# Optimization experiments

Measured on AMD Instinct MI355X. Metric: run time of the kernel, lower is better.

The kernel has to match this reference:

```python
import jax, jax.numpy as jnp
import numpy as np

G = 8          # n_games
D_IN = 512     # per-game input dim (equal for all games)
H1 = 1024
H2 = 1024
A = 128        # max_actions
B = 8192       # batch rows


def setup_inputs() -> dict:
    key = jax.random.key(0)
    ks = jax.random.split(key, 9)
    state = jax.random.normal(ks[0], (B, D_IN), dtype=jnp.float32)
    idx = jax.random.randint(ks[1], (B,), 0, G, dtype=jnp.int32)
    # per-game input linears: uniform(-1/sqrt(fan_in), 1/sqrt(fan_in))
    lim1 = 1.0 / np.sqrt(D_IN)
    W1 = jax.random.uniform(ks[2], (G, D_IN, H1), minval=-lim1, maxval=lim1, dtype=jnp.float32)
    b1 = jax.random.uniform(ks[3], (G, H1), minval=-lim1, maxval=lim1, dtype=jnp.float32)
    # shared linear
    lim2 = 1.0 / np.sqrt(H1)
    W2 = jax.random.uniform(ks[4], (H1, H2), minval=-lim2, maxval=lim2, dtype=jnp.float32)
    b2 = jax.random.uniform(ks[5], (H2,), minval=-lim2, maxval=lim2, dtype=jnp.float32)
    # per-game output heads: uniform(-0.003, 0.003)
    W3 = jax.random.uniform(ks[6], (G, H2, A), minval=-0.003, maxval=0.003, dtype=jnp.float32)
    b3 = jax.random.uniform(ks[7], (G, A), minval=-0.003, maxval=0.003, dtype=jnp.float32)
    return {"state": state, "idx": idx, "W1": W1, "b1": b1, "W2": W2, "b2": b2, "W3": W3, "b3": b3}


def reference(state, idx, W1, b1, W2, b2, W3, b3):
    # Torch code concatenates per-game groups in sorted-unique-idx order,
    # i.e. a stable permutation of rows by idx; reproduce exactly.
    perm = jnp.argsort(idx, stable=True)          # [B]
    s = state[perm]                               # [B, D_IN]
    g = idx[perm]                                 # [B] game of each permuted row
    # routed first layer: compute all games then gather per-row game
    h1_all = jnp.einsum('bd,gdh->bgh', s, W1) + b1            # [B, G, H1]
    h1 = jax.nn.relu(jnp.take_along_axis(h1_all, g[:, None, None], axis=1)[:, 0, :])  # [B, H1]
    h_f = jax.nn.relu(h1 @ W2 + b2)                            # [B, H2]
    a = jnp.tanh(jnp.einsum('bh,gha->bga', h_f, W3) + b3)      # [B, G, A]
    # NOTE: original gathers heads with the ORIGINAL (unpermuted) idx,
    # even though rows of `a` are in permuted order. Reproduce faithfully.
    out = jnp.take_along_axis(a, idx[:, None, None], axis=1)[:, 0, :]  # [B, A]
    return out
```

## Files before the change

kernel.cpp:

```cpp
#include <hip/hip_runtime.h>
#include <math.h>

#define G_GAMES 8
#define D_IN 512
#define H1 1024
#define H2 1024
#define A_DIM 128
#define B_ROWS 8192

typedef short bf16x8 __attribute__((ext_vector_type(8)));
typedef float f32x4 __attribute__((ext_vector_type(4)));

#define WS_OFF   0u
#define WS_PERM  256u
#define WS_SPERM 33280u
#define WS_W1T   (WS_SPERM + B_ROWS*D_IN*2u)
#define WS_W2T   (WS_W1T + G_GAMES*D_IN*H1*2u)
#define WS_W3T   (WS_W2T + (unsigned)H1*H2*2u)
#define WS_H1    (WS_W3T + G_GAMES*H2*A_DIM*2u)
#define WS_HF    WS_SPERM

__device__ __forceinline__ unsigned short f2bf(float x) {
  union { float f; unsigned int u; } v; v.f = x;
  unsigned int r = v.u + 0x7fffu + ((v.u >> 16) & 1u);
  return (unsigned short)(r >> 16);
}

__device__ __forceinline__ unsigned int cvt_pk_bf16(float lo, float hi) {
  unsigned int r;
  asm("v_cvt_pk_bf16_f32 %0, %1, %2" : "=v"(r) : "v"(lo), "v"(hi));
  return r;
}

__device__ __forceinline__ void async_load16(const void* gptr, void* ldsptr) {
  __builtin_amdgcn_global_load_lds(
      (const __attribute__((address_space(1))) unsigned int*)gptr,
      (__attribute__((address_space(3))) unsigned int*)ldsptr,
      16, 0, 0);
}

__device__ void sort_256(const int* __restrict__ idx, int* __restrict__ perm,
                         int* __restrict__ off) {
  __shared__ int wtot[4][9];
  __shared__ int wbase[4][9];
  __shared__ int offs[9];
  const int t = threadIdx.x, lane = t & 63, wave = t >> 6;
  int my[32];
#pragma unroll
  for (int i = 0; i < 8; ++i) {
    const int4 a = *(const int4*)(idx + t * 32 + i * 4);
    my[i*4+0] = a.x; my[i*4+1] = a.y; my[i*4+2] = a.z; my[i*4+3] = a.w;
  }
  int local[8];
#pragma unroll
  for (int g = 0; g < 8; ++g) {
    int c = 0;
#pragma unroll
    for (int i = 0; i < 32; ++i) c += (my[i] == g) ? 1 : 0;
    local[g] = c;
  }
  int incl[8];
#pragma unroll
  for (int g = 0; g < 8; ++g) {
    int v = local[g];
#pragma unroll
    for (int d = 1; d < 64; d <<= 1) {
      const int n = __shfl_up(v, d);
      if (lane >= d) v += n;
    }
    incl[g] = v;
  }
  if (lane == 63) {
#pragma unroll
    for (int g = 0; g < 8; ++g) wtot[wave][g] = incl[g];
  }
  __syncthreads();
  if (t < 8) {
    int s = 0;
#pragma unroll
    for (int w = 0; w < 4; ++w) { wbase[w][t] = s; s += wtot[w][t]; }
    wtot[0][t] = s;
  }
  __syncthreads();
  if (t == 0) {
    int s = 0;
#pragma unroll
    for (int g = 0; g < 8; ++g) { offs[g] = s; off[g] = s; s += wtot[0][g]; }
    offs[8] = s; off[8] = s;
  }
  __syncthreads();
#pragma unroll
  for (int g = 0; g < 8; ++g) {
    int sg = offs[g] + wbase[wave][g] + (incl[g] - local[g]);
#pragma unroll
    for (int i = 0; i < 32; ++i) {
      const bool m = (my[i] == g);
      if (m) perm[sg] = t * 32 + i;
      sg += m ? 1 : 0;
    }
  }
}

__device__ void trans_tile_ws(char* ldsbuf, const float* __restrict__ in,
                              unsigned short* __restrict__ out,
                              int R, int C, int xt, int yt, int z) {
  in  += (size_t)z * R * C;
  out += (size_t)z * R * C;
  unsigned short (*tl)[68] = (unsigned short(*)[68])ldsbuf;
  const int c0 = xt * 64, r0 = yt * 64;
  const int t = threadIdx.x;
#pragma unroll
  for (int pass = 0; pass < 4; ++pass) {
    const int id = pass * 256 + t;
    const int r = id >> 4, f4c = (id & 15) << 2;
    const float4 v = *(const float4*)(in + (size_t)(r0 + r) * C + c0 + f4c);
    uint2 w;
    w.x = cvt_pk_bf16(v.x, v.y);
    w.y = cvt_pk_bf16(v.z, v.w);
    *(uint2*)&tl[r][f4c] = w;
  }
  __syncthreads();
#pragma unroll
  for (int pass = 0; pass < 2; ++pass) {
    const int cc = t >> 2, k0 = ((t & 3) << 3) + (pass << 5);
    unsigned short u[8];
#pragma unroll
    for (int j = 0; j < 8; ++j) u[j] = tl[k0 + j][cc];
    uint4 v;
    v.x = (unsigned)u[0] | ((unsigned)u[1] << 16);
    v.y = (unsigned)u[2] | ((unsigned)u[3] << 16);
    v.z = (unsigned)u[4] | ((unsigned)u[5] << 16);
    v.w = (unsigned)u[6] | ((unsigned)u[7] << 16);
    *(uint4*)(out + (size_t)(c0 + cc) * R + r0 + k0) = v;
  }
}

__device__ __forceinline__ bool seg_map(const int* __restrict__ off, int T,
                                        int& g, int& seg1, int& row0) {
  int base = 0;
  for (int gg = 0; gg < 8; ++gg) {
    const int s = off[gg], e = off[gg + 1];
    const int nt = (e - s + 127) >> 7;
    if (T < base + nt) { g = gg; seg1 = e; row0 = s + (T - base) * 128; return true; }
    base += nt;
  }
  return false;
}

__device__ __forceinline__ bool seg_map32(const int* __restrict__ off, int T,
                                          int& g, int& seg1, int& row0) {
  int base = 0;
  for (int gg = 0; gg < 8; ++gg) {
    const int s = off[gg], e = off[gg + 1];
    const int nt = (e - s + 31) >> 5;
    if (T < base + nt) { g = gg; seg1 = e; row0 = s + (T - base) * 32; return true; }
    base += nt;
  }
  return false;
}

__device__ __forceinline__ void epilogue_bf16(char* smem, const f32x4 acc[4][4],
                                              const float* bj, int tid,
                                              unsigned short* __restrict__ outp,
                                              size_t ldOut, int row0, int col0,
                                              int vrows) {
  const int lane = tid & 63, wave = tid >> 6;
  const int wm = wave & 1, wn = wave >> 1;
  const int sw = lane & 15, quad = lane >> 4;
  __syncthreads();
#pragma unroll
  for (int i = 0; i < 4; ++i)
#pragma unroll
    for (int j = 0; j < 4; ++j)
#pragma unroll
      for (int r = 0; r < 4; ++r) {
        const int row = wm * 64 + i * 16 + quad * 4 + r;
        const int col = wn * 64 + j * 16 + sw;
        const float v = fmaxf(acc[i][j][r] + bj[j], 0.0f);
        *(unsigned short*)(smem + row * 264 + col * 2) = f2bf(v);
      }
  __syncthreads();
#pragma unroll
  for (int q = 0; q < 8; ++q) {
    const int idxq = q * 256 + tid;
    const int row = idxq >> 4, ch = idxq & 15;
    if (row < vrows) {
      const uint2 lo = *(const uint2*)(smem + row * 264 + ch * 16);
      const uint2 hi = *(const uint2*)(smem + row * 264 + ch * 16 + 8);
      uint4 v; v.x = lo.x; v.y = lo.y; v.z = hi.x; v.w = hi.y;
      *(uint4*)((char*)outp + ((size_t)(row0 + row) * ldOut + col0 + ch * 8) * 2) = v;
    }
  }
}

__device__ void gemm1_tile(const float* __restrict__ state,
                           const int* __restrict__ perm,
                           const unsigned short* __restrict__ W1T,
                           const float* __restrict__ b1,
                           const int* __restrict__ off,
                           unsigned short* __restrict__ h1out,
                           int T, char* smem, int tid) {
  int g, seg1, row0;
  if (!seg_map(off, T % 72, g, seg1, row0)) return;
  const int col0 = (T / 72) * 128;
  const int lane = tid & 63, wave = tid >> 6;
  const int wm = wave & 1, wn = wave >> 1;
  const int sw = lane & 15, quad = lane >> 4;
  const int lc = lane & 7;
  const int gcol = ((lane & 7) ^ (lane >> 3)) << 3;
  const float* aS[4];
  int ldsA[4];
  const unsigned short* bP[4];
#pragma unroll
  for (int c = 0; c < 4; ++c) {
    const int rl = wave * 32 + c * 8 + (lane >> 3);
    int p = row0 + rl;
    if (p > seg1 - 1) p = seg1 - 1;
    aS[c]  = state + (size_t)perm[p] * D_IN + lc * 8;
    ldsA[c] = rl * 128 + ((lc ^ (rl & 7)) << 4);
    bP[c]  = W1T + (size_t)g * H1 * D_IN + (size_t)(col0 + rl) * D_IN + gcol;
  }
  char* A0 = smem;          char* A1 = smem + 16384;
  char* B0 = smem + 32768;  char* B1 = smem + 49152;
  const int mA = wm * 64 + sw, nB = wn * 64 + sw;
  f32x4 acc[4][4] = {};
  {
    float4 t0[4], t1[4];
#pragma unroll
    for (int c = 0; c < 4; ++c) {
      t0[c] = *(const float4*)(aS[c]);
      t1[c] = *(const float4*)(aS[c] + 4);
      async_load16(bP[c], B0 + (wave * 32 + c * 8) * 128);
    }
#pragma unroll
    for (int c = 0; c < 4; ++c) {
      uint4 pk;
      pk.x = cvt_pk_bf16(t0[c].x, t0[c].y);
      pk.y = cvt_pk_bf16(t0[c].z, t0[c].w);
      pk.z = cvt_pk_bf16(t1[c].x, t1[c].y);
      pk.w = cvt_pk_bf16(t1[c].z, t1[c].w);
      *(uint4*)(A0 + ldsA[c]) = pk;
    }
  }
  const int NIT = D_IN >> 6;
#pragma unroll 2
  for (int k = 0; k < NIT; ++k) {
    __syncthreads();
    char* A = (k & 1) ? A1 : A0;
    char* B = (k & 1) ? B1 : B0;
    float4 t0[4], t1[4];
    const bool pf = (k + 1 < NIT);
    if (pf) {
      char* Bn = (k & 1) ? B0 : B1;
      const int koff = (k + 1) << 6;
#pragma unroll
      for (int c = 0; c < 4; ++c) {
        t0[c] = *(const float4*)(aS[c] + koff);
        t1[c] = *(const float4*)(aS[c] + koff + 4);
        async_load16(bP[c] + koff, Bn + (wave * 32 + c * 8) * 128);
      }
    }
#pragma unroll
    for (int ks = 0; ks < 2; ++ks) {
      const int u = ((((ks << 2) + quad) ^ (sw & 7)) << 4);
      bf16x8 aF[4], bF[4];
#pragma unroll
      for (int i = 0; i < 4; ++i) {
        aF[i] = *(const bf16x8*)(A + (mA + i * 16) * 128 + u);
        bF[i] = *(const bf16x8*)(B + (nB + i * 16) * 128 + u);
      }
#pragma unroll
      for (int i = 0; i < 4; ++i)
#pragma unroll
        for (int j = 0; j < 4; ++j)
          acc[i][j] = __builtin_amdgcn_mfma_f32_16x16x32_bf16(aF[i], bF[j], acc[i][j], 0, 0, 0);
    }
    if (pf) {
      char* An = (k & 1) ? A0 : A1;
#pragma unroll
      for (int c = 0; c < 4; ++c) {
        uint4 pk;
        pk.x = cvt_pk_bf16(t0[c].x, t0[c].y);
        pk.y = cvt_pk_bf16(t0[c].z, t0[c].w);
        pk.z = cvt_pk_bf16(t1[c].x, t1[c].y);
        pk.w = cvt_pk_bf16(t1[c].z, t1[c].w);
        *(uint4*)(An + ldsA[c]) = pk;
      }
    }
  }
  const float* bg = b1 + g * H1;
  float bj[4];
#pragma unroll
  for (int j = 0; j < 4; ++j) bj[j] = bg[col0 + wn * 64 + j * 16 + sw];
  const int vrows = min(128, seg1 - row0);
  epilogue_bf16(smem, acc, bj, tid, h1out, H1, row0, col0, vrows);
}

__device__ void gemm2_tile(const unsigned short* __restrict__ h1in,
                           const unsigned short* __restrict__ W2T,
                           const float* __restrict__ b2,
                           unsigned short* __restrict__ hfout,
                           int T, char* smem, int tid) {
  const int row0 = (T & 63) * 128, col0 = (T >> 6) * 128;
  const int lane = tid & 63, wave = tid >> 6;
  const int wm = wave & 1, wn = wave >> 1;
  const int sw = lane & 15, quad = lane >> 4;
  const int gcol = ((lane & 7) ^ (lane >> 3)) << 3;
  const unsigned short* aP[4];
  const unsigned short* bP[4];
#pragma unroll
  for (int c = 0; c < 4; ++c) {
    const int rl = wave * 32 + c * 8 + (lane >> 3);
    aP[c] = h1in + (size_t)(row0 + rl) * H1 + gcol;
    bP[c] = W2T + (size_t)(col0 + rl) * H1 + gcol;
  }
  char* A0 = smem;          char* A1 = smem + 16384;
  char* B0 = smem + 32768;  char* B1 = smem + 49152;
  const int mA = wm * 64 + sw, nB = wn * 64 + sw;
  f32x4 acc[4][4] = {};
#pragma unroll
  for (int c = 0; c < 4; ++c) {
    async_load16(aP[c], A0 + (wave * 32 + c * 8) * 128);
    async_load16(bP[c], B0 + (wave * 32 + c * 8) * 128);
  }
  const int NIT = H1 >> 6;
#pragma unroll 2
  for (int k = 0; k < NIT; ++k) {
    __syncthreads();
    char* A = (k & 1) ? A1 : A0;
    char* B = (k & 1) ? B1 : B0;
    if (k + 1 < NIT) {
      char* An = (k & 1) ? A0 : A1;
      char* Bn = (k & 1) ? B0 : B1;
      const int koff = (k + 1) << 6;
#pragma unroll
      for (int c = 0; c < 4; ++c) {
        async_load16(aP[c] + koff, An + (wave * 32 + c * 8) * 128);
        async_load16(bP[c] + koff, Bn + (wave * 32 + c * 8) * 128);
      }
    }
#pragma unroll
    for (int ks = 0; ks < 2; ++ks) {
      const int u = ((((ks << 2) + quad) ^ (sw & 7)) << 4);
      bf16x8 aF[4], bF[4];
#pragma unroll
      for (int i = 0; i < 4; ++i) {
        aF[i] = *(const bf16x8*)(A + (mA + i * 16) * 128 + u);
        bF[i] = *(const bf16x8*)(B + (nB + i * 16) * 128 + u);
      }
#pragma unroll
      for (int i = 0; i < 4; ++i)
#pragma unroll
        for (int j = 0; j < 4; ++j)
          acc[i][j] = __builtin_amdgcn_mfma_f32_16x16x32_bf16(aF[i], bF[j], acc[i][j], 0, 0, 0);
    }
  }
  float bj[4];
#pragma unroll
  for (int j = 0; j < 4; ++j) bj[j] = b2[col0 + wn * 64 + j * 16 + sw];
  epilogue_bf16(smem, acc, bj, tid, hfout, H2, row0, col0, 128);
}

__device__ void gemm3_tile(const unsigned short* __restrict__ hf,
                           const unsigned short* __restrict__ W3T,
                           const float* __restrict__ b3,
                           const int* __restrict__ off,
                           const int* __restrict__ perm,
                           float* __restrict__ outp,
                           int T, char* smem, int tid) {
  int g, seg1, row0;
  if (!seg_map32(off, T, g, seg1, row0)) return;
  const int lane = tid & 63, wave = tid >> 6;
  const int wm = wave & 1, wn = wave >> 1;
  const int sw = lane & 15, quad = lane >> 4;
  const int gcol = ((lane & 7) ^ (lane >> 3)) << 3;
  int q0 = row0 + wave * 8 + (lane >> 3);
  if (q0 > seg1 - 1) q0 = seg1 - 1;
  const unsigned short* aP = hf + (size_t)perm[q0] * H2 + gcol;
  const unsigned short* bP[4];
#pragma unroll
  for (int c = 0; c < 4; ++c) {
    const int rl = wave * 32 + c * 8 + (lane >> 3);
    bP[c] = W3T + (size_t)g * A_DIM * H2 + (size_t)rl * H2 + gcol;
  }
  char* A0 = smem;         char* A1 = smem + 4096;
  char* B0 = smem + 8192;  char* B1 = smem + 24576;
  const int mA = wm * 16 + sw;
  const int nB = wn * 64 + sw;
  f32x4 acc[4] = {};
  async_load16(aP, A0 + (wave * 8) * 128);
#pragma unroll
  for (int c = 0; c < 4; ++c)
    async_load16(bP[c], B0 + (wave * 32 + c * 8) * 128);
#pragma unroll 2
  for (int k = 0; k < (H2 >> 6); ++k) {
    __syncthreads();
    char* A = (k & 1) ? A1 : A0;
    char* B = (k & 1) ? B1 : B0;
    if (k + 1 < (H2 >> 6)) {
      char* An = (k & 1) ? A0 : A1;
      char* Bn = (k & 1) ? B0 : B1;
      const int koff = (k + 1) << 6;
      async_load16(aP + koff, An + (wave * 8) * 128);
#pragma unroll
      for (int c = 0; c < 4; ++c)
        async_load16(bP[c] + koff, Bn + (wave * 32 + c * 8) * 128);
    }
#pragma unroll
    for (int ks = 0; ks < 2; ++ks) {
      const int u = ((((ks << 2) + quad) ^ (sw & 7)) << 4);
      const bf16x8 aF = *(const bf16x8*)(A + mA * 128 + u);
      bf16x8 bF[4];
#pragma unroll
      for (int j = 0; j < 4; ++j)
        bF[j] = *(const bf16x8*)(B + (nB + j * 16) * 128 + u);
#pragma unroll
      for (int j = 0; j < 4; ++j)
        acc[j] = __builtin_amdgcn_mfma_f32_16x16x32_bf16(aF, bF[j], acc[j], 0, 0, 0);
    }
  }
  const float* bg = b3 + g * A_DIM;
  float bj[4];
#pragma unroll
  for (int j = 0; j < 4; ++j) bj[j] = bg[wn * 64 + j * 16 + sw];
  __syncthreads();
#pragma unroll
  for (int j = 0; j < 4; ++j)
#pragma unroll
    for (int r = 0; r < 4; ++r) {
      const int row = wm * 16 + quad * 4 + r;
      const int col = wn * 64 + j * 16 + sw;
      *(float*)(smem + row * 528 + col * 4) = tanhf(acc[j][r] + bj[j]);
    }
  __syncthreads();
#pragma unroll
  for (int qq = 0; qq < 4; ++qq) {
    const int idxq = qq * 256 + tid;
    const int row = idxq >> 5, ch = idxq & 31;
    if (row0 + row < seg1) {
      const uint4 v = *(const uint4*)(smem + row * 528 + ch * 16);
      *(uint4*)((char*)outp + ((size_t)perm[row0 + row] * A_DIM + ch * 4) * 4) = v;
    }
  }
}

__global__ __launch_bounds__(256) void k_pre(const float* __restrict__ W1,
                                             const int* __restrict__ idx,
                                             unsigned short* __restrict__ W1T,
                                             int* __restrict__ perm,
                                             int* __restrict__ off) {
  __shared__ __align__(16) char tsmem[8704];
  const int b = blockIdx.x;
  if (b == 0) {
    sort_256(idx, perm, off);
  } else {
    const int r0 = b - 1, z = r0 >> 7, r = r0 & 127;
    trans_tile_ws(tsmem, W1, W1T, D_IN, H1, r & 15, r >> 4, z);
  }
}

__global__ __launch_bounds__(256, 2) void k_g1(const float* __restrict__ state,
                                               const int* __restrict__ perm,
                                               const unsigned short* __restrict__ W1T,
                                               const float* __restrict__ b1,
                                               const int* __restrict__ off,
                                               const float* __restrict__ W2,
                                               const float* __restrict__ W3,
                                               unsigned short* __restrict__ W2T,
                                               unsigned short* __restrict__ W3T,
                                               unsigned short* __restrict__ h1out) {
  __shared__ __align__(16) char smem[65536];
  const int b = blockIdx.x;
  if (b >= 576) {
    const int t = b - 576;
    if (t < 256) {
      trans_tile_ws(smem, W2, W2T, H1, H2, t & 15, t >> 4, 0);
    } else {
      const int r = (t - 256) & 31, z = (t - 256) >> 5;
      trans_tile_ws(smem, W3, W3T, H2, A_DIM, r & 1, r >> 1, z);
    }
    return;
  }
  gemm1_tile(state, perm, W1T, b1, off, h1out, b, smem, threadIdx.x);
}

__global__ __launch_bounds__(256) void k_g2(const unsigned short* __restrict__ h1in,
                                            const unsigned short* __restrict__ W2T,
                                            const float* __restrict__ b2,
                                            unsigned short* __restrict__ hfout) {
  __shared__ __align__(16) char smem[65536];
  gemm2_tile(h1in, W2T, b2, hfout, blockIdx.x, smem, threadIdx.x);
}

__global__ __launch_bounds__(256) void k_g3(const unsigned short* __restrict__ hf,
                                            const unsigned short* __restrict__ W3T,
                                            const float* __restrict__ b3,
                                            const int* __restrict__ off,
                                            const int* __restrict__ perm,
                                            float* __restrict__ outp) {
  __shared__ __align__(16) char smem[40960];
  gemm3_tile(hf, W3T, b3, off, perm, outp, blockIdx.x, smem, threadIdx.x);
}

extern "C" void kernel_launch(void* const* d_in, const int* in_sizes, int n_in,
                              void* d_out, int out_size, void* d_ws, size_t ws_size,
                              hipStream_t stream) {
  (void)in_sizes; (void)n_in; (void)out_size; (void)ws_size;
  const float* state = (const float*)d_in[0];
  const int*   idx   = (const int*)d_in[1];
  const float* W1    = (const float*)d_in[2];
  const float* b1    = (const float*)d_in[3];
  const float* W2    = (const float*)d_in[4];
  const float* b2    = (const float*)d_in[5];
  const float* W3    = (const float*)d_in[6];
  const float* b3    = (const float*)d_in[7];
  float* outp = (float*)d_out;
  char* ws = (char*)d_ws;
  int* off  = (int*)(ws + WS_OFF);
  int* perm = (int*)(ws + WS_PERM);
  unsigned short* W1T   = (unsigned short*)(ws + WS_W1T);
  unsigned short* W2T   = (unsigned short*)(ws + WS_W2T);
  unsigned short* W3T   = (unsigned short*)(ws + WS_W3T);
  unsigned short* h1    = (unsigned short*)(ws + WS_H1);
  unsigned short* hf    = (unsigned short*)(ws + WS_HF);

  hipLaunchKernelGGL(k_pre, dim3(1025), dim3(256), 0, stream,
                     W1, idx, W1T, perm, off);
  hipLaunchKernelGGL(k_g1, dim3(1088), dim3(256), 0, stream,
                     state, perm, W1T, b1, off, W2, W3, W2T, W3T, h1);
  hipLaunchKernelGGL(k_g2, dim3(512), dim3(256), 0, stream, h1, W2T, b2, hf);
  hipLaunchKernelGGL(k_g3, dim3(264), dim3(256), 0, stream, hf, W3T, b3, off, perm, outp);
}
```

Baseline: 154.3 us.

## Single-buffer GEMM2 LDS to raise occupancy to three blocks per CU

The shared-layer GEMM kernel is inlined and changed from double-buffered LDS (64 KB) to a single buffer (about 33 KB), with launch bounds asking for 3 blocks per CU. Each iteration now loads a tile, syncs, then computes, so loads no longer overlap the MFMAs within a block. The intent is to hide that latency through more resident blocks per CU instead. The cost is two barriers per k-step, plus possible register pressure from the occupancy hint.

```diff
diff --git a/kernel.cpp b/kernel.cpp
--- a/kernel.cpp
+++ b/kernel.cpp
@@ -294,71 +294,6 @@
   for (int j = 0; j < 4; ++j) bj[j] = bg[col0 + wn * 64 + j * 16 + sw];
   const int vrows = min(128, seg1 - row0);
   epilogue_bf16(smem, acc, bj, tid, h1out, H1, row0, col0, vrows);
-}
-
-__device__ void gemm2_tile(const unsigned short* __restrict__ h1in,
-                           const unsigned short* __restrict__ W2T,
-                           const float* __restrict__ b2,
-                           unsigned short* __restrict__ hfout,
-                           int T, char* smem, int tid) {
-  const int row0 = (T & 63) * 128, col0 = (T >> 6) * 128;
-  const int lane = tid & 63, wave = tid >> 6;
-  const int wm = wave & 1, wn = wave >> 1;
-  const int sw = lane & 15, quad = lane >> 4;
-  const int gcol = ((lane & 7) ^ (lane >> 3)) << 3;
-  const unsigned short* aP[4];
-  const unsigned short* bP[4];
-#pragma unroll
-  for (int c = 0; c < 4; ++c) {
-    const int rl = wave * 32 + c * 8 + (lane >> 3);
-    aP[c] = h1in + (size_t)(row0 + rl) * H1 + gcol;
-    bP[c] = W2T + (size_t)(col0 + rl) * H1 + gcol;
-  }
-  char* A0 = smem;          char* A1 = smem + 16384;
-  char* B0 = smem + 32768;  char* B1 = smem + 49152;
-  const int mA = wm * 64 + sw, nB = wn * 64 + sw;
-  f32x4 acc[4][4] = {};
-#pragma unroll
-  for (int c = 0; c < 4; ++c) {
-    async_load16(aP[c], A0 + (wave * 32 + c * 8) * 128);
-    async_load16(bP[c], B0 + (wave * 32 + c * 8) * 128);
-  }
-  const int NIT = H1 >> 6;
-#pragma unroll 2
-  for (int k = 0; k < NIT; ++k) {
-    __syncthreads();
-    char* A = (k & 1) ? A1 : A0;
-    char* B = (k & 1) ? B1 : B0;
-    if (k + 1 < NIT) {
-      char* An = (k & 1) ? A0 : A1;
-      char* Bn = (k & 1) ? B0 : B1;
-      const int koff = (k + 1) << 6;
-#pragma unroll
-      for (int c = 0; c < 4; ++c) {
-        async_load16(aP[c] + koff, An + (wave * 32 + c * 8) * 128);
-        async_load16(bP[c] + koff, Bn + (wave * 32 + c * 8) * 128);
-      }
-    }
-#pragma unroll
-    for (int ks = 0; ks < 2; ++ks) {
-      const int u = ((((ks << 2) + quad) ^ (sw & 7)) << 4);
-      bf16x8 aF[4], bF[4];
-#pragma unroll
-      for (int i = 0; i < 4; ++i) {
-        aF[i] = *(const bf16x8*)(A + (mA + i * 16) * 128 + u);
-        bF[i] = *(const bf16x8*)(B + (nB + i * 16) * 128 + u);
-      }
-#pragma unroll
-      for (int i = 0; i < 4; ++i)
-#pragma unroll
-        for (int j = 0; j < 4; ++j)
-          acc[i][j] = __builtin_amdgcn_mfma_f32_16x16x32_bf16(aF[i], bF[j], acc[i][j], 0, 0, 0);
-    }
-  }
-  float bj[4];
-#pragma unroll
-  for (int j = 0; j < 4; ++j) bj[j] = b2[col0 + wn * 64 + j * 16 + sw];
-  epilogue_bf16(smem, acc, bj, tid, hfout, H2, row0, col0, 128);
 }
 
 __device__ void gemm3_tile(const unsigned short* __restrict__ hf,
@@ -484,12 +419,60 @@
   gemm1_tile(state, perm, W1T, b1, off, h1out, b, smem, threadIdx.x);
 }
 
-__global__ __launch_bounds__(256) void k_g2(const unsigned short* __restrict__ h1in,
-                                            const unsigned short* __restrict__ W2T,
-                                            const float* __restrict__ b2,
-                                            unsigned short* __restrict__ hfout) {
-  __shared__ __align__(16) char smem[65536];
-  gemm2_tile(h1in, W2T, b2, hfout, blockIdx.x, smem, threadIdx.x);
+__global__ __launch_bounds__(256, 3) void k_g2(const unsigned short* __restrict__ h1in,
+                                               const unsigned short* __restrict__ W2T,
+                                               const float* __restrict__ b2,
+                                               unsigned short* __restrict__ hfout) {
+  __shared__ __align__(16) char smem[33792];
+  const int T = blockIdx.x, tid = threadIdx.x;
+  const int row0 = (T & 63) * 128, col0 = (T >> 6) * 128;
+  const int lane = tid & 63, wave = tid >> 6;
+  const int wm = wave & 1, wn = wave >> 1;
+  const int sw = lane & 15, quad = lane >> 4;
+  const int gcol = ((lane & 7) ^ (lane >> 3)) << 3;
+  const unsigned short* aP[4];
+  const unsigned short* bP[4];
+#pragma unroll
+  for (int c = 0; c < 4; ++c) {
+    const int rl = wave * 32 + c * 8 + (lane >> 3);
+    aP[c] = h1in + (size_t)(row0 + rl) * H1 + gcol;
+    bP[c] = W2T + (size_t)(col0 + rl) * H1 + gcol;
+  }
+  char* A = smem;
+  char* B = smem + 16384;
+  const int mA = wm * 64 + sw, nB = wn * 64 + sw;
+  f32x4 acc[4][4] = {};
+  const int NIT = H1 >> 6;
+#pragma unroll 2
+  for (int k = 0; k < NIT; ++k) {
+    if (k) __syncthreads();
+    const int koff = k << 6;
+#pragma unroll
+    for (int c = 0; c < 4; ++c) {
+      async_load16(aP[c] + koff, A + (wave * 32 + c * 8) * 128);
+      async_load16(bP[c] + koff, B + (wave * 32 + c * 8) * 128);
+    }
+    __syncthreads();
+#pragma unroll
+    for (int ks = 0; ks < 2; ++ks) {
+      const int u = ((((ks << 2) + quad) ^ (sw & 7)) << 4);
+      bf16x8 aF[4], bF[4];
+#pragma unroll
+      for (int i = 0; i < 4; ++i) {
+        aF[i] = *(const bf16x8*)(A + (mA + i * 16) * 128 + u);
+        bF[i] = *(const bf16x8*)(B + (nB + i * 16) * 128 + u);
+      }
+#pragma unroll
+      for (int i = 0; i < 4; ++i)
+#pragma unroll
+        for (int j = 0; j < 4; ++j)
+          acc[i][j] = __builtin_amdgcn_mfma_f32_16x16x32_bf16(aF[i], bF[j], acc[i][j], 0, 0, 0);
+    }
+  }
+  float bj[4];
+#pragma unroll
+  for (int j = 0; j < 4; ++j) bj[j] = b2[col0 + wn * 64 + j * 16 + sw];
+  epilogue_bf16(smem, acc, bj, tid, hfout, H2, row0, col0, 128);
 }
 
 __global__ __launch_bounds__(256) void k_g3(const unsigned short* __restrict__ hf,
```

Measured after the change: 156.5 us. No clear change (+1.4%).
